# Kernel optimization log

Hardware: AMD Instinct MI355X
Metric: run time of the kernel (lower is better)

Reference implementation:

```python
import jax, jax.numpy as jnp
import numpy as np

DIM = 256
HEADS = 8
G = 8            # group (window) size per axis
POS_DIM = 16     # (dim // 4) // 4
MLP_HIDDEN = 4 * DIM


def layernorm(x, g, b, eps=1e-5):
    m = x.mean(-1, keepdims=True)
    v = ((x - m) ** 2).mean(-1, keepdims=True)
    return (x - m) / jnp.sqrt(v + eps) * g + b


def setup_inputs() -> dict:
    key = jax.random.key(0)
    ks = jax.random.split(key, 32)
    s = 0.02
    d = {}
    d['x'] = jax.random.normal(ks[0], (1, 32768, DIM), jnp.float32)
    d['y'] = jax.random.normal(ks[1], (1, 32768, DIM), jnp.float32)
    d['n1_g'] = jnp.ones((DIM,), jnp.float32)
    d['n1_b'] = jnp.zeros((DIM,), jnp.float32)
    d['qkv_w'] = jax.random.normal(ks[2], (DIM, 3 * DIM), jnp.float32) * s
    d['qkv_b'] = jnp.zeros((3 * DIM,), jnp.float32)
    d['pp_w'] = jax.random.normal(ks[3], (3, POS_DIM), jnp.float32) * s
    d['pp_b'] = jnp.zeros((POS_DIM,), jnp.float32)
    d['p1_lng'] = jnp.ones((POS_DIM,), jnp.float32)
    d['p1_lnb'] = jnp.zeros((POS_DIM,), jnp.float32)
    d['p1_w'] = jax.random.normal(ks[4], (POS_DIM, POS_DIM), jnp.float32) * s
    d['p1_b'] = jnp.zeros((POS_DIM,), jnp.float32)
    d['p2_lng'] = jnp.ones((POS_DIM,), jnp.float32)
    d['p2_lnb'] = jnp.zeros((POS_DIM,), jnp.float32)
    d['p2_w'] = jax.random.normal(ks[5], (POS_DIM, POS_DIM), jnp.float32) * s
    d['p2_b'] = jnp.zeros((POS_DIM,), jnp.float32)
    d['p3_lng'] = jnp.ones((POS_DIM,), jnp.float32)
    d['p3_lnb'] = jnp.zeros((POS_DIM,), jnp.float32)
    d['p3_w'] = jax.random.normal(ks[6], (POS_DIM, HEADS), jnp.float32) * s
    d['p3_b'] = jnp.zeros((HEADS,), jnp.float32)
    d['proj_w'] = jax.random.normal(ks[7], (DIM, DIM), jnp.float32) * s
    d['proj_b'] = jnp.zeros((DIM,), jnp.float32)
    d['n2_g'] = jnp.ones((DIM,), jnp.float32)
    d['n2_b'] = jnp.zeros((DIM,), jnp.float32)
    d['fc1_w'] = jax.random.normal(ks[8], (DIM, MLP_HIDDEN), jnp.float32) * s
    d['fc1_b'] = jnp.zeros((MLP_HIDDEN,), jnp.float32)
    d['fc2_w'] = jax.random.normal(ks[9], (MLP_HIDDEN, DIM), jnp.float32) * s
    d['fc2_b'] = jnp.zeros((DIM,), jnp.float32)
    d['H'] = 32
    d['W'] = 32
    d['D'] = 32
    return d


def reference(x, y, n1_g, n1_b, qkv_w, qkv_b, pp_w, pp_b,
              p1_lng, p1_lnb, p1_w, p1_b, p2_lng, p2_lnb, p2_w, p2_b,
              p3_lng, p3_lnb, p3_w, p3_b, proj_w, proj_b,
              n2_g, n2_b, fc1_w, fc1_b, fc2_w, fc2_b, H, W, D):
    B, L, C = x.shape
    nh, g = HEADS, G
    hd = C // nh
    shortcut = x
    xn = layernorm(x, n1_g, n1_b)
    xv = xn.reshape(B, H, W, D, C)
    yv = y.reshape(B, H, W, D, C)  # note: y is NOT normed in the original

    # SDA window partition (H,W,D divisible by g -> no padding, zero mask)
    def part(t):
        t = t.reshape(B, H // g, g, W // g, g, D // g, g, C)
        t = t.transpose(0, 1, 3, 5, 2, 4, 6, 7)
        return t.reshape(-1, g * g * g, C)

    xg, yg = part(xv), part(yv)
    B_, N, _ = xg.shape

    # original quirk: self.qkv used for BOTH x and y (qkv_y layer unused)
    qkv = (xg @ qkv_w + qkv_b).reshape(B_, N, 3, nh, hd).transpose(2, 0, 3, 1, 4)
    qkv_y = (yg @ qkv_w + qkv_b).reshape(B_, N, 3, nh, hd).transpose(2, 0, 3, 1, 4)
    q = qkv[0] * (hd ** -0.5)
    k_y, v_y = qkv_y[1], qkv_y[2]

    attn = jnp.einsum('bhnd,bhmd->bhnm', q, k_y)  # [B_, nh, N, N]

    # dynamic relative position bias (small MLP + gather)
    rng = jnp.arange(1 - g, g)
    bh, bw, bd = jnp.meshgrid(rng, rng, rng, indexing='ij')
    biases = jnp.stack([bh, bw, bd], -1).reshape(-1, 3).astype(x.dtype)  # [(2g-1)^3, 3]
    pos = biases @ pp_w + pp_b
    pos = jax.nn.relu(layernorm(pos, p1_lng, p1_lnb)) @ p1_w + p1_b
    pos = jax.nn.relu(layernorm(pos, p2_lng, p2_lnb)) @ p2_w + p2_b
    pos = jax.nn.relu(layernorm(pos, p3_lng, p3_lnb)) @ p3_w + p3_b  # [(2g-1)^3, nh]

    c = jnp.arange(g)
    ch, cw, cd = jnp.meshgrid(c, c, c, indexing='ij')
    cf = jnp.stack([ch, cw, cd], 0).reshape(3, -1)          # [3, g^3]
    rel = (cf[:, :, None] - cf[:, None, :]).transpose(1, 2, 0) + (g - 1)
    idx = rel[..., 0] * (2 * g - 1) * (2 * g - 1) + rel[..., 1] * (2 * g - 1) + rel[..., 2]
    bias = pos[idx].transpose(2, 0, 1)  # [nh, N, N]

    attn = jax.nn.softmax(attn + bias[None], axis=-1)
    out = jnp.einsum('bhnm,bhmd->bhnd', attn, v_y).transpose(0, 2, 1, 3).reshape(B_, N, C)
    out = out @ proj_w + proj_b

    # reverse window partition
    out = out.reshape(B, H // g, W // g, D // g, g, g, g, C)
    out = out.transpose(0, 1, 4, 2, 5, 3, 6, 7).reshape(B, H * W * D, C)

    x = shortcut + out
    x2 = layernorm(x, n2_g, n2_b)
    h = jax.nn.gelu(x2 @ fc1_w + fc1_b, approximate=False)
    x = x + (h @ fc2_w + fc2_b)
    return x
```

## Files before the change

### kernel.cpp

```cpp
#include <hip/hip_runtime.h>
#include <cstdint>
#include <cstddef>

typedef unsigned int u32;
typedef unsigned short u16;
typedef __attribute__((ext_vector_type(8))) short bf16x8;
typedef __attribute__((ext_vector_type(4))) float f32x4;

#define DEV __device__ __forceinline__

DEV u16 f2b(float f){ u32 x = __float_as_uint(f); x += 0x7fffu + ((x>>16)&1u); return (u16)(x>>16); }
DEV u32 pk2(float a, float b){
  u32 r;
  asm("v_cvt_pk_bf16_f32 %0, %1, %2" : "=v"(r) : "v"(a), "v"(b));
  return r;
}

DEV void gll16(const void* g, void* l){
  __builtin_amdgcn_global_load_lds((const __attribute__((address_space(1))) u32*)g,
                                   (__attribute__((address_space(3))) u32*)l, 16, 0, 0);
}

DEV void win_n(int r, int& win, int& n){
  int d_ = r & 31, w_ = (r>>5)&31, h_ = r>>10;
  win = ((h_>>3)<<4) | ((w_>>3)<<2) | (d_>>3);
  n   = ((h_&7)<<6)  | ((w_&7)<<3)  | (d_&7);
}
DEV int tok_of(int r){
  int win = r>>9, nn = r&511;
  int bh = win>>4, bw=(win>>2)&3, bd=win&3;
  int ih = nn>>6,  iw=(nn>>3)&7,  id=nn&7;
  return ((bh*8+ih)<<10) | ((bw*8+iw)<<5) | (bd*8+id);
}


__global__ void wtrall_k(const float* __restrict__ qkv_w, const float* __restrict__ proj_w,
                         const float* __restrict__ fc1_w, const float* __restrict__ fc2_w,
                         u16* __restrict__ qkvT, u16* __restrict__ projT,
                         u16* __restrict__ fc1T, u16* __restrict__ fc2T){
  int f = blockIdx.x*256 + threadIdx.x;
  const float* w; u16* wt; int g; bool k10 = false; int N;
  if (f < 196608)      { w=qkv_w;  wt=qkvT;  g=f;        N=768;  }
  else if (f < 262144) { w=proj_w; wt=projT; g=f-196608; N=256;  }
  else if (f < 524288) { w=fc1_w;  wt=fc1T;  g=f-262144; N=1024; }
  else                 { w=fc2_w;  wt=fc2T;  g=f-524288; N=256;  k10=true; }
  int n = k10 ? (g>>10) : (g>>8);
  int k = k10 ? (g&1023) : (g&255);
  wt[g] = f2b(w[(size_t)k*N + n]);
}

template<int NOUT>
DEV void pstage(float* v, const float* g, const float* b, const float* W, const float* bb){
  float m = 0.f;
  #pragma unroll
  for (int i=0;i<16;i++) m += v[i];
  m *= 0.0625f;
  float q = 0.f;
  #pragma unroll
  for (int i=0;i<16;i++){ float d=v[i]-m; q += d*d; }
  float rs = rsqrtf(q*0.0625f + 1e-5f);
  float u[16];
  #pragma unroll
  for (int i=0;i<16;i++){ float t = (v[i]-m)*rs*g[i] + b[i]; u[i] = t>0.f?t:0.f; }
  #pragma unroll
  for (int o=0;o<NOUT;o++){
    float s = bb[o];
    #pragma unroll
    for (int kk=0;kk<16;kk++) s += u[kk]*W[kk*NOUT+o];
    v[o] = s;
  }
}

__global__ void posmlp_k(const float* pp_w, const float* pp_b,
                         const float* g1, const float* b1, const float* w1, const float* bb1,
                         const float* g2, const float* b2, const float* w2, const float* bb2,
                         const float* g3, const float* b3, const float* w3, const float* bb3,
                         float* __restrict__ posb){
  int i = blockIdx.x*256 + threadIdx.x;
  if (i >= 3375) return;
  int t = i;
  int bd = t % 15; t /= 15;
  int bw = t % 15; t /= 15;
  int bh = t;
  float fh = (float)(bh-7), fw = (float)(bw-7), fd = (float)(bd-7);
  float v[16];
  #pragma unroll
  for (int o=0;o<16;o++) v[o] = fh*pp_w[o] + fw*pp_w[16+o] + fd*pp_w[32+o] + pp_b[o];
  pstage<16>(v, g1,b1,w1,bb1);
  pstage<16>(v, g2,b2,w2,bb2);
  pstage<8> (v, g3,b3,w3,bb3);
  #pragma unroll
  for (int h=0;h<8;h++) posb[(size_t)h*3376 + i] = v[h] * 1.4426950408889634f;
}

struct GemmP {
  const u16* A;
  const float* Af32;
  const float* lng; const float* lnb;
  const u16* Bt;
  int K;
  const float* bvec;
  float scale;
  const float* add32;
  float* out32;
  u16* out16;
  u16* out16b;
};

template<int MODE>
DEV void epi(const GemmP& p, int r, int c, float val){
  if constexpr (MODE==0){
    float qv = (val + p.bvec[c]) * p.scale;
    int win, n; win_n(r, win, n);
    int hh = c>>5, dd = c&31;
    p.out16[((size_t)((win*8+hh)*512 + n)<<5) + dd] = f2b(qv);
  } else if constexpr (MODE==1){
    float ov = val + p.bvec[c];
    int win, n; win_n(r, win, n);
    int cc = c & 255;
    int hh = cc>>5, dd = cc&31;
    size_t base = (size_t)(win*8+hh)*16384;
    if (c < 256){
      int nc = n>>4, ln2 = ((dd>>3)<<4)|(n&15), jj = dd&7;
      p.out16[base + (size_t)(nc*64+ln2)*8 + jj] = f2b(ov);
    } else {
      int fi = ((n>>5)<<1) | (dd>>4);
      int ln2 = (((n>>3)&3)<<4)|(dd&15), jj = n&7;
      p.out16b[base + (size_t)(fi*64+ln2)*8 + jj] = f2b(ov);
    }
  } else if constexpr (MODE==2){
    int l = tok_of(r);
    size_t o = (size_t)l*256 + c;
    p.out32[o] = val + p.bvec[c] + p.add32[o];
  } else if constexpr (MODE==3){
    float u = val + p.bvec[c];
    float e = exp2f(u*(2.3022083f + 0.1029437f*u*u));
    float ge = u*e*__builtin_amdgcn_rcpf(e+1.f);
    p.out16[(size_t)r*1024 + c] = f2b(ge);
  } else {
    size_t o = (size_t)r*256 + c;
    p.out32[o] = val + p.bvec[c] + p.add32[o];
  }
}

template<int MODE, int NT, int STG>
__global__ __launch_bounds__(512, 2)
void gemmA_k(GemmP p){
  __shared__ u16 lA[16384];
  __shared__ u16 lB[3][4096];
  const int tid = threadIdx.x;
  const int wid = tid>>6, lane = tid&63;
  const int lr = lane&15, lg = lane>>4;
  const int m0 = blockIdx.x*64;
  const int wm = (wid>>2)*32, wn = (wid&3)*32;
  const int T = NT*8;
  const f32x4 z4 = {0.f,0.f,0.f,0.f};

  if constexpr (STG==3){
    #pragma unroll
    for (int it=0; it<4; ++it){
      int f = it*8 + wid;
      int rt = f>>3, kt = f&7;
      int row = m0 + rt*16 + lr;
      const u16* ga = p.A + ((size_t)((row>>9)*8 + kt)*512 + (row&511))*32 + lg*8;
      gll16(ga, (char*)lA + f*1024 + lane*16);
    }
  } else {
    const int row = wid*8 + (lane>>3);
    const int sub = lane&7;
    const float* src = p.Af32 + (size_t)(m0+row)*256;
    float xv[32];
    #pragma unroll
    for (int j=0;j<8;j++){
      float4 v = *(const float4*)(src + j*32 + sub*4);
      xv[j*4+0]=v.x; xv[j*4+1]=v.y; xv[j*4+2]=v.z; xv[j*4+3]=v.w;
    }
    float mu=0.f, rs=1.f;
    if constexpr (STG==1){
      float s=0.f;
      #pragma unroll
      for (int i2=0;i2<32;i2++) s += xv[i2];
      s += __shfl_xor(s,1); s += __shfl_xor(s,2); s += __shfl_xor(s,4);
      mu = s*(1.f/256.f);
      float q2=0.f;
      #pragma unroll
      for (int i2=0;i2<32;i2++){ float d=xv[i2]-mu; q2 += d*d; }
      q2 += __shfl_xor(q2,1); q2 += __shfl_xor(q2,2); q2 += __shfl_xor(q2,4);
      rs = rsqrtf(q2*(1.f/256.f) + 1e-5f);
    }
    const int rt = wid>>1, q = (wid&1)*8 + (lane>>3);
    #pragma unroll
    for (int j=0;j<8;j++){
      float o0,o1,o2,o3;
      if constexpr (STG==1){
        float4 gg = *(const float4*)(p.lng + j*32 + sub*4);
        float4 bb = *(const float4*)(p.lnb + j*32 + sub*4);
        o0=(xv[j*4+0]-mu)*rs*gg.x+bb.x; o1=(xv[j*4+1]-mu)*rs*gg.y+bb.y;
        o2=(xv[j*4+2]-mu)*rs*gg.z+bb.z; o3=(xv[j*4+3]-mu)*rs*gg.w+bb.w;
      } else {
        o0=xv[j*4+0]; o1=xv[j*4+1]; o2=xv[j*4+2]; o3=xv[j*4+3];
      }
      int f = rt*8 + j;
      *(uint2*)((char*)lA + f*1024 + (sub>>1)*256 + q*16 + (sub&1)*8)
          = make_uint2((u32)f2b(o0) | ((u32)f2b(o1)<<16),
                       (u32)f2b(o2) | ((u32)f2b(o3)<<16));
    }
    asm volatile("s_waitcnt lgkmcnt(0)" ::: "memory");
  }
  auto stageB = [&](int buf, int t){
    int j = t>>3, kt = t&7;
    gll16(p.Bt + (size_t)(j*128 + wid*16 + lr)*256 + kt*32 + lg*8,
          (char*)lB[buf] + wid*1024 + lane*16);
  };
  stageB(0, 0);
  if (T > 1) stageB(1, 1);

  f32x4 acc[2][2];
  #pragma unroll
  for (int i=0;i<2;i++){ acc[i][0]=z4; acc[i][1]=z4; }

  int cur = 0, stg = 2;
  for (int t=0; t<T; ++t){
    const int kt = t&7;
    if (t+1 >= T)          asm volatile("s_waitcnt vmcnt(0)"  ::: "memory");
    else if (kt==0 && t)   asm volatile("s_waitcnt vmcnt(17)" ::: "memory");
    else                   asm volatile("s_waitcnt vmcnt(1)"  ::: "memory");
    __builtin_amdgcn_s_barrier();
    __builtin_amdgcn_sched_barrier(0);
    bf16x8 af[2], bfr[2];
    #pragma unroll
    for (int i=0;i<2;i++){
      int fA = ((wid>>2)*2 + i)*8 + kt;
      af[i] = *(const bf16x8*)((const char*)lA + fA*1024 + lane*16);
    }
    #pragma unroll
    for (int j=0;j<2;j++){
      int fB = (wid&3)*2 + j;
      bfr[j] = *(const bf16x8*)((const char*)lB[cur] + fB*1024 + lane*16);
    }
    #pragma unroll
    for (int i=0;i<2;i++)
      #pragma unroll
      for (int j=0;j<2;j++)
        acc[i][j] = __builtin_amdgcn_mfma_f32_16x16x32_bf16(af[i], bfr[j], acc[i][j], 0,0,0);
    __builtin_amdgcn_sched_barrier(0);
    if (kt == 7){
      int n0 = (t>>3)*128;
      #pragma unroll
      for (int i=0;i<2;i++)
        #pragma unroll
        for (int j=0;j<2;j++){
          #pragma unroll
          for (int v=0;v<4;v++)
            epi<MODE>(p, m0 + wm + i*16 + lg*4 + v, n0 + wn + j*16 + lr, acc[i][j][v]);
          acc[i][j] = z4;
        }
    }
    if (t+2 < T) stageB(stg, t+2);
    cur = (cur==2)?0:cur+1;
    stg = (stg==2)?0:stg+1;
  }
}

__global__ __launch_bounds__(512, 2)
void gemmW_k(GemmP p){
  __shared__ u16 lA[3][2048];
  __shared__ u16 lB[3][8192];
  const int tid = threadIdx.x;
  const int wid = tid>>6, lane = tid&63;
  const int lr = lane&15, lg = lane>>4;
  const int m0 = blockIdx.x*64;
  const int wm = (wid>>2)*32, wn = (wid&3)*64;
  const f32x4 z4 = {0.f,0.f,0.f,0.f};

  auto stage = [&](int buf, int kt){
    {
      int f = wid>>1, half = wid&1;
      if (lane < 32){
        int lg2 = half*2 + (lane>>4);
        gll16(p.A + (size_t)(m0 + f*16 + (lane&15))*1024 + kt*32 + lg2*8,
              (char*)lA[buf] + f*1024 + half*512 + lane*16);
      }
    }
    #pragma unroll
    for (int r=0;r<2;r++){
      int fb = wid*2 + r;
      gll16(p.Bt + (size_t)(fb*16 + lr)*1024 + kt*32 + lg*8,
            (char*)lB[buf] + fb*1024 + lane*16);
    }
  };
  stage(0, 0);
  stage(1, 1);

  f32x4 acc[2][4];
  #pragma unroll
  for (int i=0;i<2;i++)
    #pragma unroll
    for (int j=0;j<4;j++) acc[i][j] = z4;

  int cur = 0, stg = 2;
  for (int kt=0; kt<32; ++kt){
    if (kt+1 < 32) asm volatile("s_waitcnt vmcnt(3)" ::: "memory");
    else           asm volatile("s_waitcnt vmcnt(0)" ::: "memory");
    __builtin_amdgcn_s_barrier();
    __builtin_amdgcn_sched_barrier(0);
    bf16x8 af[2], bfr[4];
    #pragma unroll
    for (int i=0;i<2;i++){
      int fA = (wid>>2)*2 + i;
      af[i] = *(const bf16x8*)((const char*)lA[cur] + fA*1024 + lane*16);
    }
    #pragma unroll
    for (int j=0;j<4;j++){
      int fB = (wid&3)*4 + j;
      bfr[j] = *(const bf16x8*)((const char*)lB[cur] + fB*1024 + lane*16);
    }
    #pragma unroll
    for (int i=0;i<2;i++)
      #pragma unroll
      for (int j=0;j<4;j++)
        acc[i][j] = __builtin_amdgcn_mfma_f32_16x16x32_bf16(af[i], bfr[j], acc[i][j], 0,0,0);
    __builtin_amdgcn_sched_barrier(0);
    if (kt+2 < 32) stage(stg, kt+2);
    cur = (cur==2)?0:cur+1;
    stg = (stg==2)?0:stg+1;
  }

  #pragma unroll
  for (int i=0;i<2;i++)
    #pragma unroll
    for (int j=0;j<4;j++)
      #pragma unroll
      for (int v=0;v<4;v++)
        epi<4>(p, m0 + wm + i*16 + lg*4 + v, wn + j*16 + lr, acc[i][j][v]);
}

__global__ __launch_bounds__(512, 2)
void attn_k(const u16* __restrict__ Q, const u16* __restrict__ Kf,
            const u16* __restrict__ Vf, const float* __restrict__ posb,
            u16* __restrict__ outF){
  __shared__ u16 lK[16384];
  __shared__ u16 lV[16384];
  __shared__ float lPf[3392];
  const int bid = blockIdx.x;
  const int hh = bid&7;
  const int tid = threadIdx.x, wid = tid>>6, lane = tid&63;
  const int lr = lane&15, lg = lane>>4;
  const u16* Kb = Kf + (size_t)bid*16384;
  const u16* Vb = Vf + (size_t)bid*16384;
  const u16* Qb = Q  + (size_t)bid*16384;
  #pragma unroll
  for (int r=0;r<4;r++){
    int off = (r*512 + tid)*16;
    gll16((const char*)Kb + off, (char*)lK + off);
    gll16((const char*)Vb + off, (char*)lV + off);
  }
  const float* ptab = posb + (size_t)hh*3376;
  for (int t=tid; t<3375; t+=512) lPf[t] = ptab[t];
  __syncthreads();
  const f32x4 z4 = {0.f,0.f,0.f,0.f};
  const bf16x8 ones = {(short)0x3F80,(short)0x3F80,(short)0x3F80,(short)0x3F80,
                       (short)0x3F80,(short)0x3F80,(short)0x3F80,(short)0x3F80};

  for (int ch=0; ch<4; ++ch){
    const int r0 = wid*64 + ch*16;
    const int q  = r0 + lr;
    const int Ab = (q>>6)*225 + ((q>>3)&7)*15 + (q&7) + 1687 - (lg>>1)*15 - (lg&1)*4;
    bf16x8 qf = *(const bf16x8*)(Qb + (size_t)q*32 + lg*8);
    f32x4 o0 = z4, o1 = z4, as_ = z4;
    #pragma unroll
    for (int ph=0; ph<2; ++ph){
      f32x4 sf[16];
      __builtin_amdgcn_s_setprio(1);
      #pragma unroll
      for (int i=0;i<16;i++){
        int nc = ph*16 + i;
        bf16x8 kf = *(const bf16x8*)&lK[(nc*64 + lane)*8];
        sf[i] = __builtin_amdgcn_mfma_f32_16x16x32_bf16(kf, qf, z4, 0,0,0);
      }
      __builtin_amdgcn_s_setprio(0);
      #pragma unroll
      for (int i=0;i<16;i++){
        int nc = ph*16 + i;
        const float* bp = lPf + (Ab - (nc>>2)*225 - (nc&3)*30 - 3);
        sf[i][3] = exp2f(sf[i][3] + bp[0]);
        sf[i][2] = exp2f(sf[i][2] + bp[1]);
        sf[i][1] = exp2f(sf[i][1] + bp[2]);
        sf[i][0] = exp2f(sf[i][0] + bp[3]);
      }
      #pragma unroll
      for (int kc=0;kc<8;kc++){
        u32 a0 = pk2(sf[2*kc  ][0], sf[2*kc  ][1]);
        u32 a1 = pk2(sf[2*kc  ][2], sf[2*kc  ][3]);
        u32 b0 = pk2(sf[2*kc+1][0], sf[2*kc+1][1]);
        u32 b1 = pk2(sf[2*kc+1][2], sf[2*kc+1][3]);
        asm("v_permlane32_swap_b32 %0, %1" : "+v"(a0), "+v"(b0));
        asm("v_permlane16_swap_b32 %0, %1" : "+v"(a0), "+v"(b0));
        asm("v_permlane32_swap_b32 %0, %1" : "+v"(a1), "+v"(b1));
        asm("v_permlane16_swap_b32 %0, %1" : "+v"(a1), "+v"(b1));
        bf16x8 pf;
        ((u32*)&pf)[0]=a0; ((u32*)&pf)[1]=a1; ((u32*)&pf)[2]=b0; ((u32*)&pf)[3]=b1;
        int kcg = ph*8 + kc;
        bf16x8 v0 = *(const bf16x8*)&lV[(size_t)((kcg*2+0)*64 + lane)*8];
        bf16x8 v1 = *(const bf16x8*)&lV[(size_t)((kcg*2+1)*64 + lane)*8];
        __builtin_amdgcn_s_setprio(1);
        o0  = __builtin_amdgcn_mfma_f32_16x16x32_bf16(pf, v0, o0, 0,0,0);
        o1  = __builtin_amdgcn_mfma_f32_16x16x32_bf16(pf, v1, o1, 0,0,0);
        as_ = __builtin_amdgcn_mfma_f32_16x16x32_bf16(pf, ones, as_, 0,0,0);
        __builtin_amdgcn_s_setprio(0);
      }
    }
    #pragma unroll
    for (int v=0;v<4;v++){
      float inv = 1.0f / as_[v];
      int n = r0 + lg*4 + v;
      size_t base = ((size_t)bid*512 + n)*32;
      outF[base + lr]      = f2b(o0[v]*inv);
      outF[base + 16 + lr] = f2b(o1[v]*inv);
    }
  }
}

extern "C" void kernel_launch(void* const* d_in, const int* in_sizes, int n_in,
                              void* d_out, int out_size, void* d_ws, size_t ws_size,
                              hipStream_t stream){
  const float* x      = (const float*)d_in[0];
  const float* y      = (const float*)d_in[1];
  const float* n1_g   = (const float*)d_in[2];
  const float* n1_b   = (const float*)d_in[3];
  const float* qkv_w  = (const float*)d_in[4];
  const float* qkv_b  = (const float*)d_in[5];
  const float* pp_w   = (const float*)d_in[6];
  const float* pp_b   = (const float*)d_in[7];
  const float* p1_lng = (const float*)d_in[8];
  const float* p1_lnb = (const float*)d_in[9];
  const float* p1_w   = (const float*)d_in[10];
  const float* p1_b   = (const float*)d_in[11];
  const float* p2_lng = (const float*)d_in[12];
  const float* p2_lnb = (const float*)d_in[13];
  const float* p2_w   = (const float*)d_in[14];
  const float* p2_b   = (const float*)d_in[15];
  const float* p3_lng = (const float*)d_in[16];
  const float* p3_lnb = (const float*)d_in[17];
  const float* p3_w   = (const float*)d_in[18];
  const float* p3_b   = (const float*)d_in[19];
  const float* proj_w = (const float*)d_in[20];
  const float* proj_b = (const float*)d_in[21];
  const float* n2_g   = (const float*)d_in[22];
  const float* n2_b   = (const float*)d_in[23];
  const float* fc1_w  = (const float*)d_in[24];
  const float* fc1_b  = (const float*)d_in[25];
  const float* fc2_w  = (const float*)d_in[26];
  const float* fc2_b  = (const float*)d_in[27];
  float* out = (float*)d_out;
  char* ws = (char*)d_ws;

  u16*   qkvT  = (u16*)  (ws + 0);
  u16*   projT = (u16*)  (ws + 393216);
  u16*   fc1T  = (u16*)  (ws + 524288);
  u16*   fc2T  = (u16*)  (ws + 1048576);
  float* posb  = (float*)(ws + 1572864);
  u16*   hbuf  = (u16*)  (ws + 5898240);
  u16*   Qb    = (u16*)  (ws + 39452672);
  u16*   Kfb   = (u16*)  (ws + 56229888);
  u16*   Vfb   = (u16*)  (ws + 73007104);
  u16*   attnF = (u16*)  (ws + 89784320);
  float* xres  = (float*)(ws + 106561536);

  wtrall_k<<<3072,256,0,stream>>>(qkv_w, proj_w, fc1_w, fc2_w, qkvT, projT, fc1T, fc2T);
  posmlp_k<<<14,256,0,stream>>>(pp_w, pp_b,
                                p1_lng,p1_lnb,p1_w,p1_b,
                                p2_lng,p2_lnb,p2_w,p2_b,
                                p3_lng,p3_lnb,p3_w,p3_b, posb);

  GemmP pq; pq.A=nullptr; pq.Af32=x; pq.lng=n1_g; pq.lnb=n1_b;
  pq.Bt=qkvT; pq.K=256; pq.bvec=qkv_b;
  pq.scale=0.17677669529663687f*1.4426950408889634f;
  pq.add32=nullptr; pq.out32=nullptr; pq.out16=Qb; pq.out16b=nullptr;
  gemmA_k<0,2,1><<<512,512,0,stream>>>(pq);

  GemmP pkv; pkv.A=nullptr; pkv.Af32=y; pkv.lng=nullptr; pkv.lnb=nullptr;
  pkv.Bt=qkvT + 256*256; pkv.K=256; pkv.bvec=qkv_b + 256;
  pkv.scale=1.f; pkv.add32=nullptr; pkv.out32=nullptr; pkv.out16=Kfb; pkv.out16b=Vfb;
  gemmA_k<1,4,2><<<512,512,0,stream>>>(pkv);

  attn_k<<<512,512,0,stream>>>(Qb, Kfb, Vfb, posb, attnF);

  GemmP pp; pp.A=attnF; pp.Af32=nullptr; pp.lng=nullptr; pp.lnb=nullptr;
  pp.Bt=projT; pp.K=256; pp.bvec=proj_b;
  pp.scale=1.f; pp.add32=x; pp.out32=xres; pp.out16=nullptr; pp.out16b=nullptr;
  gemmA_k<2,2,3><<<512,512,0,stream>>>(pp);

  GemmP pf1; pf1.A=nullptr; pf1.Af32=xres; pf1.lng=n2_g; pf1.lnb=n2_b;
  pf1.Bt=fc1T; pf1.K=256; pf1.bvec=fc1_b;
  pf1.scale=1.f; pf1.add32=nullptr; pf1.out32=nullptr; pf1.out16=hbuf; pf1.out16b=nullptr;
  gemmA_k<3,8,1><<<512,512,0,stream>>>(pf1);

  GemmP pf2; pf2.A=hbuf; pf2.Af32=nullptr; pf2.lng=nullptr; pf2.lnb=nullptr;
  pf2.Bt=fc2T; pf2.K=1024; pf2.bvec=fc2_b;
  pf2.scale=1.f; pf2.add32=xres; pf2.out32=out; pf2.out16=nullptr; pf2.out16b=nullptr;
  gemmW_k<<<512,512,0,stream>>>(pf2);
}
```

Baseline: 246.7 us.

## Keep A fragments in registers, reuse LDS for B; fold bias into MFMA accumulator

```diff
diff --git a/kernel.cpp b/kernel.cpp
--- a/kernel.cpp
+++ b/kernel.cpp
@@ -143,11 +143,10 @@
   }
 }
 
-template<int MODE, int NT, int STG>
+template<int MODE, int STG, int NT>
 __global__ __launch_bounds__(512, 2)
 void gemmA_k(GemmP p){
-  __shared__ u16 lA[16384];
-  __shared__ u16 lB[3][4096];
+  __shared__ u16 smem[16384];
   const int tid = threadIdx.x;
   const int wid = tid>>6, lane = tid&63;
   const int lr = lane&15, lg = lane>>4;
@@ -162,9 +161,11 @@
       int f = it*8 + wid;
       int rt = f>>3, kt = f&7;
       int row = m0 + rt*16 + lr;
-      const u16* ga = p.A + ((size_t)((row>>9)*8 + kt)*512 + (row&511))*32 + lg*8;
-      gll16(ga, (char*)lA + f*1024 + lane*16);
-    }
+      gll16(p.A + ((size_t)((row>>9)*8 + kt)*512 + (row&511))*32 + lg*8,
+            (char*)smem + f*1024 + lane*16);
+    }
+    asm volatile("s_waitcnt vmcnt(0)" ::: "memory");
+    __builtin_amdgcn_s_barrier();
   } else {
     const int row = wid*8 + (lane>>3);
     const int sub = lane&7;
@@ -201,64 +202,73 @@
         o0=xv[j*4+0]; o1=xv[j*4+1]; o2=xv[j*4+2]; o3=xv[j*4+3];
       }
       int f = rt*8 + j;
-      *(uint2*)((char*)lA + f*1024 + (sub>>1)*256 + q*16 + (sub&1)*8)
+      *(uint2*)((char*)smem + f*1024 + (sub>>1)*256 + q*16 + (sub&1)*8)
           = make_uint2((u32)f2b(o0) | ((u32)f2b(o1)<<16),
                        (u32)f2b(o2) | ((u32)f2b(o3)<<16));
     }
     asm volatile("s_waitcnt lgkmcnt(0)" ::: "memory");
-  }
+    __builtin_amdgcn_s_barrier();
+  }
+  bf16x8 areg[2][8];
+  #pragma unroll
+  for (int i=0;i<2;i++)
+    #pragma unroll
+    for (int kt=0;kt<8;kt++){
+      int f = ((wid>>2)*2 + i)*8 + kt;
+      areg[i][kt] = *(const bf16x8*)((const char*)smem + f*1024 + lane*16);
+    }
+  asm volatile("s_waitcnt lgkmcnt(0)" ::: "memory");
+  __builtin_amdgcn_s_barrier();
+
+  u16* lB = smem;
   auto stageB = [&](int buf, int t){
     int j = t>>3, kt = t&7;
     gll16(p.Bt + (size_t)(j*128 + wid*16 + lr)*256 + kt*32 + lg*8,
-          (char*)lB[buf] + wid*1024 + lane*16);
+          (char*)lB + buf*8192 + wid*1024 + lane*16);
   };
   stageB(0, 0);
   if (T > 1) stageB(1, 1);
 
+  constexpr int EPIW = (MODE==2) ? 33 : 17;
   f32x4 acc[2][2];
   #pragma unroll
   for (int i=0;i<2;i++){ acc[i][0]=z4; acc[i][1]=z4; }
 
-  int cur = 0, stg = 2;
-  for (int t=0; t<T; ++t){
-    const int kt = t&7;
-    if (t+1 >= T)          asm volatile("s_waitcnt vmcnt(0)"  ::: "memory");
-    else if (kt==0 && t)   asm volatile("s_waitcnt vmcnt(17)" ::: "memory");
-    else                   asm volatile("s_waitcnt vmcnt(1)"  ::: "memory");
-    __builtin_amdgcn_s_barrier();
-    __builtin_amdgcn_sched_barrier(0);
-    bf16x8 af[2], bfr[2];
-    #pragma unroll
-    for (int i=0;i<2;i++){
-      int fA = ((wid>>2)*2 + i)*8 + kt;
-      af[i] = *(const bf16x8*)((const char*)lA + fA*1024 + lane*16);
-    }
-    #pragma unroll
-    for (int j=0;j<2;j++){
-      int fB = (wid&3)*2 + j;
-      bfr[j] = *(const bf16x8*)((const char*)lB[cur] + fB*1024 + lane*16);
-    }
-    #pragma unroll
-    for (int i=0;i<2;i++)
-      #pragma unroll
-      for (int j=0;j<2;j++)
-        acc[i][j] = __builtin_amdgcn_mfma_f32_16x16x32_bf16(af[i], bfr[j], acc[i][j], 0,0,0);
-    __builtin_amdgcn_sched_barrier(0);
-    if (kt == 7){
-      int n0 = (t>>3)*128;
+  int cur = 0, stg = 2, t = 0;
+  for (int j=0; j<NT; ++j){
+    #pragma unroll
+    for (int kt=0; kt<8; ++kt, ++t){
+      if (t+1 >= T)        asm volatile("s_waitcnt vmcnt(0)" ::: "memory");
+      else if (kt==0 && t) asm volatile("s_waitcnt vmcnt(%0)" :: "i"(EPIW) : "memory");
+      else                 asm volatile("s_waitcnt vmcnt(1)" ::: "memory");
+      __builtin_amdgcn_s_barrier();
+      __builtin_amdgcn_sched_barrier(0);
+      bf16x8 bfr[2];
+      #pragma unroll
+      for (int jj=0;jj<2;jj++)
+        bfr[jj] = *(const bf16x8*)((const char*)lB + cur*8192 + ((wid&3)*2+jj)*1024 + lane*16);
       #pragma unroll
       for (int i=0;i<2;i++)
         #pragma unroll
-        for (int j=0;j<2;j++){
+        for (int jj=0;jj<2;jj++)
+          acc[i][jj] = __builtin_amdgcn_mfma_f32_16x16x32_bf16(areg[i][kt], bfr[jj], acc[i][jj], 0,0,0);
+      __builtin_amdgcn_sched_barrier(0);
+      if (kt == 7){
+        int n0 = j*128;
+        #pragma unroll
+        for (int i=0;i<2;i++)
           #pragma unroll
-          for (int v=0;v<4;v++)
-            epi<MODE>(p, m0 + wm + i*16 + lg*4 + v, n0 + wn + j*16 + lr, acc[i][j][v]);
-          acc[i][j] = z4;
-        }
-    }
-    if (t+2 < T) stageB(stg, t+2);
-    cur = (cur==2)?0:cur+1;
-    stg = (stg==2)?0:stg+1;
+          for (int jj=0;jj<2;jj++){
+            #pragma unroll
+            for (int v=0;v<4;v++)
+              epi<MODE>(p, m0 + wm + i*16 + lg*4 + v, n0 + wn + jj*16 + lr, acc[i][jj][v]);
+            acc[i][jj] = z4;
+          }
+      }
+      if (t+2 < T) stageB(stg, t+2);
+      cur = (cur==2)?0:cur+1;
+      stg = (stg==2)?0:stg+1;
+    }
   }
 }
 
@@ -375,18 +385,18 @@
       #pragma unroll
       for (int i=0;i<16;i++){
         int nc = ph*16 + i;
+        const float* bp = lPf + (Ab - (nc>>2)*225 - (nc&3)*30 - 3);
+        f32x4 c; c[0]=bp[3]; c[1]=bp[2]; c[2]=bp[1]; c[3]=bp[0];
         bf16x8 kf = *(const bf16x8*)&lK[(nc*64 + lane)*8];
-        sf[i] = __builtin_amdgcn_mfma_f32_16x16x32_bf16(kf, qf, z4, 0,0,0);
+        sf[i] = __builtin_amdgcn_mfma_f32_16x16x32_bf16(kf, qf, c, 0,0,0);
       }
       __builtin_amdgcn_s_setprio(0);
       #pragma unroll
       for (int i=0;i<16;i++){
-        int nc = ph*16 + i;
-        const float* bp = lPf + (Ab - (nc>>2)*225 - (nc&3)*30 - 3);
-        sf[i][3] = exp2f(sf[i][3] + bp[0]);
-        sf[i][2] = exp2f(sf[i][2] + bp[1]);
-        sf[i][1] = exp2f(sf[i][1] + bp[2]);
-        sf[i][0] = exp2f(sf[i][0] + bp[3]);
+        sf[i][0] = exp2f(sf[i][0]);
+        sf[i][1] = exp2f(sf[i][1]);
+        sf[i][2] = exp2f(sf[i][2]);
+        sf[i][3] = exp2f(sf[i][3]);
       }
       #pragma unroll
       for (int kc=0;kc<8;kc++){
@@ -477,24 +487,24 @@
   pq.Bt=qkvT; pq.K=256; pq.bvec=qkv_b;
   pq.scale=0.17677669529663687f*1.4426950408889634f;
   pq.add32=nullptr; pq.out32=nullptr; pq.out16=Qb; pq.out16b=nullptr;
-  gemmA_k<0,2,1><<<512,512,0,stream>>>(pq);
+  gemmA_k<0,1,2><<<512,512,0,stream>>>(pq);
 
   GemmP pkv; pkv.A=nullptr; pkv.Af32=y; pkv.lng=nullptr; pkv.lnb=nullptr;
   pkv.Bt=qkvT + 256*256; pkv.K=256; pkv.bvec=qkv_b + 256;
   pkv.scale=1.f; pkv.add32=nullptr; pkv.out32=nullptr; pkv.out16=Kfb; pkv.out16b=Vfb;
-  gemmA_k<1,4,2><<<512,512,0,stream>>>(pkv);
+  gemmA_k<1,2,4><<<512,512,0,stream>>>(pkv);
 
   attn_k<<<512,512,0,stream>>>(Qb, Kfb, Vfb, posb, attnF);
 
   GemmP pp; pp.A=attnF; pp.Af32=nullptr; pp.lng=nullptr; pp.lnb=nullptr;
   pp.Bt=projT; pp.K=256; pp.bvec=proj_b;
   pp.scale=1.f; pp.add32=x; pp.out32=xres; pp.out16=nullptr; pp.out16b=nullptr;
-  gemmA_k<2,2,3><<<512,512,0,stream>>>(pp);
+  gemmA_k<2,3,2><<<512,512,0,stream>>>(pp);
 
   GemmP pf1; pf1.A=nullptr; pf1.Af32=xres; pf1.lng=n2_g; pf1.lnb=n2_b;
   pf1.Bt=fc1T; pf1.K=256; pf1.bvec=fc1_b;
   pf1.scale=1.f; pf1.add32=nullptr; pf1.out32=nullptr; pf1.out16=hbuf; pf1.out16b=nullptr;
-  gemmA_k<3,8,1><<<512,512,0,stream>>>(pf1);
+  gemmA_k<3,1,8><<<512,512,0,stream>>>(pf1);
 
   GemmP pf2; pf2.A=hbuf; pf2.Af32=nullptr; pf2.lng=nullptr; pf2.lnb=nullptr;
   pf2.Bt=fc2T; pf2.K=1024; pf2.bvec=fc2_b;
```

New measurement: 252.2 us. +2.2%, slower.
